# Kernel optimization log

Measured on AMD Instinct MI355X. Metric: run time of the kernel, lower is better.

Reference implementation:

```python
import jax, jax.numpy as jnp
import numpy as np

AH, AW = 8, 8            # aligned_height, aligned_width
SCALE = 0.0625           # spatial_scale = 1/16
IMG = 1024               # image size implied by 64x64 feature map at stride 16


def setup_inputs() -> dict:
    key = jax.random.key(0)
    k1, k2, k3, k4, k5 = jax.random.split(key, 5)
    B, C, H, W = 4, 256, 64, 64
    N = 2000
    features = jax.random.normal(k1, (B, C, H, W), dtype=jnp.float32)
    # ROIs: (batch_idx, x1, y1, x2, y2) in image coordinates
    bidx = jax.random.randint(k2, (N,), 0, B).astype(jnp.float32)
    cx = jax.random.uniform(k3, (N,), minval=0.0, maxval=IMG)
    cy = jax.random.uniform(k4, (N,), minval=0.0, maxval=IMG)
    wh = jax.random.uniform(k5, (N, 2), minval=32.0, maxval=512.0)
    x1 = jnp.clip(cx - wh[:, 0] / 2, 0.0, IMG - 1.0)
    y1 = jnp.clip(cy - wh[:, 1] / 2, 0.0, IMG - 1.0)
    x2 = jnp.clip(cx + wh[:, 0] / 2, x1 + 16.0, float(IMG))
    y2 = jnp.clip(cy + wh[:, 1] / 2, y1 + 16.0, float(IMG))
    rois = jnp.stack([bidx, x1, y1, x2, y2], axis=1).astype(jnp.float32)
    return {"features": features, "rois": rois}


def _roi_align(features, rois):
    # Classic RoIAlign (crop_and_resize style): one bilinear sample per output
    # cell, sample grid spans the ROI with (aligned-1) intervals.
    B, C, H, W = features.shape
    N = rois.shape[0]
    b = rois[:, 0].astype(jnp.int32)
    x1 = rois[:, 1] * SCALE
    y1 = rois[:, 2] * SCALE
    x2 = rois[:, 3] * SCALE
    y2 = rois[:, 4] * SCALE
    bin_h = (y2 - y1) / (AH - 1.0)
    bin_w = (x2 - x1) / (AW - 1.0)
    ys = y1[:, None, None] + bin_h[:, None, None] * jnp.arange(AH, dtype=jnp.float32)[None, :, None]
    xs = x1[:, None, None] + bin_w[:, None, None] * jnp.arange(AW, dtype=jnp.float32)[None, None, :]
    ys = jnp.broadcast_to(ys, (N, AH, AW))
    xs = jnp.broadcast_to(xs, (N, AH, AW))
    valid = (ys >= 0) & (ys < H) & (xs >= 0) & (xs < W)
    y0 = jnp.floor(ys)
    x0 = jnp.floor(xs)
    ly = ys - y0  # bilinear weights
    lx = xs - x0
    iy0 = jnp.clip(y0.astype(jnp.int32), 0, H - 1)
    ix0 = jnp.clip(x0.astype(jnp.int32), 0, W - 1)
    iy1 = jnp.clip(iy0 + 1, 0, H - 1)
    ix1 = jnp.clip(ix0 + 1, 0, W - 1)
    bb = b[:, None, None]

    def g(iy, ix):
        return features[bb, :, iy, ix]  # [N, AH, AW, C]

    ly_ = ly[..., None]
    lx_ = lx[..., None]
    v = ((1 - ly_) * (1 - lx_) * g(iy0, ix0)
         + (1 - ly_) * lx_ * g(iy0, ix1)
         + ly_ * (1 - lx_) * g(iy1, ix0)
         + ly_ * lx_ * g(iy1, ix1))
    v = jnp.where(valid[..., None], v, 0.0)
    return jnp.transpose(v, (0, 3, 1, 2))  # [N, C, AH, AW]


def _max_pool_2x2_s1(x):
    # max_pool2d(kernel_size=2, stride=1): [N,C,h,w] -> [N,C,h-1,w-1]
    return jnp.maximum(
        jnp.maximum(x[:, :, :-1, :-1], x[:, :, :-1, 1:]),
        jnp.maximum(x[:, :, 1:, :-1], x[:, :, 1:, 1:]),
    )


def reference(features, rois):
    x = _roi_align(features, rois)
    return _max_pool_2x2_s1(x)  # [N, C, AH-1, AW-1]
```

## Files before the change

kernel.cpp:

```cpp
#include <hip/hip_runtime.h>
#include <cstdint>

constexpr int CCH = 256;
constexpr int HH  = 64;
constexpr int WW  = 64;
constexpr int OHW = 49;
constexpr float RSCALE = 0.0625f;

#define FMUL __fmul_rn
#define FADD __fadd_rn
#define FSUB __fsub_rn
#define FDIV __fdiv_rn

typedef float     v4f __attribute__((ext_vector_type(4)));
typedef _Float16  h2  __attribute__((ext_vector_type(2)));
typedef _Float16  h4  __attribute__((ext_vector_type(4)));

__device__ __forceinline__ h2 pkrtz(float a, float b) {
  auto t = __builtin_amdgcn_cvt_pkrtz(a, b);
  union { decltype(t) s; h2 d; } c; c.s = t; return c.d;
}
__device__ __forceinline__ h4 bcast4(float a) {
  h2 t = pkrtz(a, a);
  return __builtin_shufflevector(t, t, 0, 1, 0, 1);
}
__device__ __forceinline__ h4 u2h(uint2 u) {
  union { uint2 u; h4 h; } c; c.u = u; return c.h;
}
__device__ __forceinline__ h4 h4max(h4 a, h4 b) {
  return __builtin_elementwise_max(a, b);
}

__global__ __launch_bounds__(256) void ktrans_sched(const float* __restrict__ in,
                                                    unsigned short* __restrict__ out,
                                                    const float* __restrict__ rois,
                                                    int N, int slots, int do_sched,
                                                    int B, int* __restrict__ meta) {
  const int t = threadIdx.x;

  if ((int)blockIdx.z == B) {
    if (blockIdx.x != 0 || blockIdx.y != 0 || !do_sched) return;
    __shared__ int cnt[4], rnk[4], off[4], slack[4], excess[4];
    if (t < 4) { cnt[t] = 0; rnk[t] = 0; }
    __syncthreads();
    for (int i = t; i < N; i += 256) atomicAdd(&cnt[(int)rois[i * 5]], 1);
    __syncthreads();
    if (t == 0) {
      int o = 0, cs = 0, ce = 0;
      for (int p = 0; p < 4; ++p) {
        off[p] = o; o += cnt[p];
        slack[p]  = cs; if (slots - cnt[p] > 0) cs += slots - cnt[p];
        excess[p] = ce; if (cnt[p] - slots > 0) ce += cnt[p] - slots;
        meta[p] = cnt[p]; meta[4 + p] = off[p]; meta[8 + p] = slack[p];
      }
    }
    __syncthreads();
    int* perm = meta + 16;
    for (int i = t; i < N; i += 256) {
      const int b = (int)rois[i * 5];
      perm[off[b] + atomicAdd(&rnk[b], 1)] = i;
    }
    __syncthreads();
    int* extra = meta + 16 + N;
    for (int p = 0; p < 4; ++p) {
      const int ex = cnt[p] - slots;
      for (int e = t; e < ex; e += 256) extra[excess[p] + e] = perm[off[p] + slots + e];
    }
    return;
  }

  __shared__ float tile[64][65];
  const int b  = blockIdx.z;
  const int c0 = blockIdx.y * 64;
  const int s0 = blockIdx.x * 64;
  const float* inb = in + (size_t)b * CCH * (HH * WW);
  unsigned short* outb = out + (size_t)b * (HH * WW) * CCH;

  const int cl = t >> 4, sq = t & 15;
#pragma unroll
  for (int k = 0; k < 4; ++k) {
    const int c = cl + 16 * k;
    const v4f v = __builtin_nontemporal_load(
        (const v4f*)(inb + (size_t)(c0 + c) * (HH * WW) + s0 + 4 * sq));
    tile[c][4 * sq + 0] = v[0];
    tile[c][4 * sq + 1] = v[1];
    tile[c][4 * sq + 2] = v[2];
    tile[c][4 * sq + 3] = v[3];
  }
  __syncthreads();
  const int cq = t & 15, rl = t >> 4;
#pragma unroll
  for (int k = 0; k < 4; ++k) {
    const int r = rl + 16 * k;
    union { h2 h; unsigned u; } p0, p1;
    p0.h.x = (_Float16)tile[4 * cq + 0][r];
    p0.h.y = (_Float16)tile[4 * cq + 1][r];
    p1.h.x = (_Float16)tile[4 * cq + 2][r];
    p1.h.y = (_Float16)tile[4 * cq + 3][r];
    uint2 w; w.x = p0.u; w.y = p1.u;
    *(uint2*)(outb + (size_t)(s0 + r) * CCH + c0 + 4 * cq) = w;
  }
}

__global__ __launch_bounds__(256, 4) void roi_kernel12(const uint2* __restrict__ feat,
                                                       const float* __restrict__ rois,
                                                       const int* __restrict__ meta,
                                                       int N, int M, int use_perm,
                                                       float* __restrict__ out) {
  __shared__ __attribute__((aligned(16))) h4       ldsA[OHW * 32];
  __shared__ __attribute__((aligned(16))) _Float16 ldsC[(CCH / 2) * OHW];
  const int t = threadIdx.x;
  const int g = t & 31;
  const int r = t >> 5;

  const int c0_ = use_perm ? meta[0] : 0;
  const int c1_ = use_perm ? meta[1] : 0;
  const int c2_ = use_perm ? meta[2] : 0;
  const int c3_ = use_perm ? meta[3] : 0;
  const int o0_ = use_perm ? meta[4] : 0, o1_ = use_perm ? meta[5] : 0;
  const int o2_ = use_perm ? meta[6] : 0, o3_ = use_perm ? meta[7] : 0;
  const int s0_ = use_perm ? meta[8] : 0, s1_ = use_perm ? meta[9] : 0;
  const int s2_ = use_perm ? meta[10] : 0, s3_ = use_perm ? meta[11] : 0;
  const int* perm  = meta + 16;
  const int* extra = meta + 16 + N;

  for (int i = blockIdx.x; i < M; i += gridDim.x) {
    int n, half;
    if (use_perm) {
      const int p = (i & 7) >> 1;
      half        = i & 1;
      const int s = i >> 3;
      const int c_ = p == 0 ? c0_ : (p == 1 ? c1_ : (p == 2 ? c2_ : c3_));
      const int o_ = p == 0 ? o0_ : (p == 1 ? o1_ : (p == 2 ? o2_ : o3_));
      const int sl = p == 0 ? s0_ : (p == 1 ? s1_ : (p == 2 ? s2_ : s3_));
      n = (s < c_) ? perm[o_ + s] : extra[sl + (s - c_)];
    } else {
      n = i >> 1; half = i & 1;
    }

    const float rb = rois[n * 5 + 0];
    const float x1 = FMUL(rois[n * 5 + 1], RSCALE);
    const float y1 = FMUL(rois[n * 5 + 2], RSCALE);
    const float x2 = FMUL(rois[n * 5 + 3], RSCALE);
    const float y2 = FMUL(rois[n * 5 + 4], RSCALE);
    const int   b  = (int)rb;
    const float bh = FDIV(FSUB(y2, y1), 7.0f);
    const float bw = FDIV(FSUB(x2, x1), 7.0f);

    int   xo0[8], xo1[8];
    float lx[8];
    bool  xv[8];
#pragma unroll
    for (int q = 0; q < 8; ++q) {
      const float xs = FADD(x1, FMUL(bw, (float)q));
      xv[q] = (xs >= 0.0f) && (xs < (float)WW);
      const float xf = floorf(xs);
      lx[q] = FSUB(xs, xf);
      int a = (int)xf;
      a = a < 0 ? 0 : (a > WW - 1 ? WW - 1 : a);
      xo0[q] = a * (CCH / 4);
      xo1[q] = ((a + 1 > WW - 1) ? WW - 1 : a + 1) * (CCH / 4);
    }

    const float ys = FADD(y1, FMUL(bh, (float)r));
    const bool  yv = (ys >= 0.0f) && (ys < (float)HH);
    const float yf = floorf(ys);
    const float ly = FSUB(ys, yf);
    int d = (int)yf;
    d = d < 0 ? 0 : (d > HH - 1 ? HH - 1 : d);
    const int d1 = (d + 1 > HH - 1) ? HH - 1 : d + 1;

    const uint2* fb = feat + (size_t)b * (HH * WW) * (CCH / 4) + (half * 32 + g);
    const uint2* r0 = fb + (size_t)d  * (WW * (CCH / 4));
    const uint2* r1 = fb + (size_t)d1 * (WW * (CCH / 4));
    const float wy1 = ly, wy0 = 1.0f - ly;

    uint2 g00[8], g01[8], g10[8], g11[8];
#pragma unroll
    for (int q = 0; q < 8; ++q) {
      g00[q] = r0[xo0[q]];
      g01[q] = r0[xo1[q]];
      g10[q] = r1[xo0[q]];
      g11[q] = r1[xo1[q]];
    }

    h4 hc[7], vprev;
#pragma unroll
    for (int h = 0; h < 2; ++h) {
      h4 v[4];
#pragma unroll
      for (int q = 0; q < 4; ++q) {
        const int s = 4 * h + q;
        const bool ok = yv && xv[s];
        const float wx1 = lx[s], wx0 = 1.0f - wx1;
        const h4 w00 = bcast4(wy0 * wx0);
        const h4 w01 = bcast4(wy0 * wx1);
        const h4 w10 = bcast4(wy1 * wx0);
        const h4 w11 = bcast4(wy1 * wx1);
        h4 rr = w00 * u2h(g00[s]) + w01 * u2h(g01[s])
              + w10 * u2h(g10[s]) + w11 * u2h(g11[s]);
        v[q] = ok ? rr : h4{};
      }
      if (h == 0) {
        hc[0] = h4max(v[0], v[1]);
        hc[1] = h4max(v[1], v[2]);
        hc[2] = h4max(v[2], v[3]);
        vprev = v[3];
      } else {
        hc[3] = h4max(vprev, v[0]);
        hc[4] = h4max(v[0], v[1]);
        hc[5] = h4max(v[1], v[2]);
        hc[6] = h4max(v[2], v[3]);
      }
    }

    if (r >= 1) {
#pragma unroll
      for (int m = 0; m < 7; ++m)
        ldsA[((r - 1) * 7 + m) * 32 + g] = hc[m];
    }
    __syncthreads();

    if (r <= 6) {
      _Float16* cb = ldsC + (4 * g) * OHW + r * 7;
#pragma unroll
      for (int m = 0; m < 7; ++m) {
        const h4 x = h4max(hc[m], ldsA[(r * 7 + m) * 32 + g]);
        cb[0 * OHW + m] = x[0];
        cb[1 * OHW + m] = x[1];
        cb[2 * OHW + m] = x[2];
        cb[3 * OHW + m] = x[3];
      }
    }
    __syncthreads();

    const uint2* cs = (const uint2*)ldsC;
    v4f* o4 = (v4f*)(out + (size_t)n * (CCH * OHW) + half * (CCH / 2) * OHW);
#pragma unroll
    for (int m = 0; m < 7; ++m) {
      const int idx = m * 256 + t;
      if (idx < (CCH / 2) * OHW / 4) {
        const uint2 qv = cs[idx];
        union { unsigned u; h2 h; } e0, e1;
        e0.u = qv.x; e1.u = qv.y;
        v4f wv;
        wv.x = (float)e0.h.x;
        wv.y = (float)e0.h.y;
        wv.z = (float)e1.h.x;
        wv.w = (float)e1.h.y;
        __builtin_nontemporal_store(wv, o4 + idx);
      }
    }
  }
}

__global__ __launch_bounds__(256) void roi_kernel_fb(const float* __restrict__ feat,
                                                     const float* __restrict__ rois,
                                                     float* __restrict__ out) {
  __shared__ float sout[CCH * OHW];
  const int n = blockIdx.x;
  const int c = threadIdx.x;

  const float rb = rois[n * 5 + 0];
  const float x1 = FMUL(rois[n * 5 + 1], RSCALE);
  const float y1 = FMUL(rois[n * 5 + 2], RSCALE);
  const float x2 = FMUL(rois[n * 5 + 3], RSCALE);
  const float y2 = FMUL(rois[n * 5 + 4], RSCALE);
  const int b = (int)rb;
  const float bh = FDIV(FSUB(y2, y1), 7.0f);
  const float bw = FDIV(FSUB(x2, x1), 7.0f);

  int ix0[8], ix1[8], iy0[8], iy1[8];
  float lx[8], ly[8];
  bool xv[8], yv[8];
#pragma unroll
  for (int i = 0; i < 8; ++i) {
    const float xs = FADD(x1, FMUL(bw, (float)i));
    const float ys = FADD(y1, FMUL(bh, (float)i));
    xv[i] = (xs >= 0.0f) && (xs < (float)WW);
    yv[i] = (ys >= 0.0f) && (ys < (float)HH);
    const float xf = floorf(xs);
    const float yf = floorf(ys);
    lx[i] = FSUB(xs, xf);
    ly[i] = FSUB(ys, yf);
    int a = (int)xf;
    a = a < 0 ? 0 : (a > WW - 1 ? WW - 1 : a);
    ix0[i] = a;
    ix1[i] = (a + 1 > WW - 1) ? WW - 1 : a + 1;
    int d = (int)yf;
    d = d < 0 ? 0 : (d > HH - 1 ? HH - 1 : d);
    iy0[i] = d;
    iy1[i] = (d + 1 > HH - 1) ? HH - 1 : d + 1;
  }

  const float* fbp = feat + ((size_t)b * CCH + c) * (size_t)(HH * WW);
  float hp[7];
#pragma unroll
  for (int j = 0; j < 8; ++j) {
    float v[8];
    const float wy1 = ly[j], wy0 = 1.0f - ly[j];
#pragma unroll
    for (int i = 0; i < 8; ++i) {
      if (yv[j] && xv[i]) {
        const float f00 = fbp[iy0[j] * WW + ix0[i]];
        const float f01 = fbp[iy0[j] * WW + ix1[i]];
        const float f10 = fbp[iy1[j] * WW + ix0[i]];
        const float f11 = fbp[iy1[j] * WW + ix1[i]];
        const float wx1 = lx[i], wx0 = 1.0f - wx1;
        v[i] = wy0 * (wx0 * f00 + wx1 * f01) + wy1 * (wx0 * f10 + wx1 * f11);
      } else {
        v[i] = 0.0f;
      }
    }
    float hc[7];
#pragma unroll
    for (int i = 0; i < 7; ++i) hc[i] = fmaxf(v[i], v[i + 1]);
    if (j > 0) {
#pragma unroll
      for (int i = 0; i < 7; ++i)
        sout[c * OHW + (j - 1) * 7 + i] = fmaxf(hp[i], hc[i]);
    }
#pragma unroll
    for (int i = 0; i < 7; ++i) hp[i] = hc[i];
  }
  __syncthreads();
  const float4* s4 = (const float4*)sout;
  float4* o4 = (float4*)(out + (size_t)n * (CCH * OHW));
  for (int q = c; q < (CCH * OHW) / 4; q += 256) o4[q] = s4[q];
}

extern "C" void kernel_launch(void* const* d_in, const int* in_sizes, int n_in,
                              void* d_out, int out_size, void* d_ws, size_t ws_size,
                              hipStream_t stream) {
  (void)n_in; (void)out_size;
  const float* feat = (const float*)d_in[0];
  const float* rois = (const float*)d_in[1];
  float* out = (float*)d_out;
  const int N = in_sizes[1] / 5;
  const int B = in_sizes[0] / (CCH * HH * WW);
  const int M = 2 * N;
  const size_t featbf_bytes = (size_t)in_sizes[0] * sizeof(unsigned short);
  const size_t meta_bytes   = (size_t)(16 + 2 * N) * sizeof(int);

  if (ws_size >= featbf_bytes + meta_bytes) {
    unsigned short* featbf = (unsigned short*)d_ws;
    int* meta = (int*)((char*)d_ws + featbf_bytes);
    const int use_perm = (B == 4 && (M & 7) == 0) ? 1 : 0;

    ktrans_sched<<<dim3((HH * WW) / 64, CCH / 64, B + 1), dim3(256), 0, stream>>>(
        feat, featbf, rois, N, M >> 3, use_perm, B, meta);
    const int grid = (M >= 2048) ? 2048 : M;
    roi_kernel12<<<dim3(grid), dim3(256), 0, stream>>>(
        (const uint2*)featbf, rois, meta, N, M, use_perm, out);
  } else {
    roi_kernel_fb<<<dim3(N), dim3(256), 0, stream>>>(feat, rois, out);
  }
}
```

Baseline: 133.1 us.

## Fuse transpose, scheduling and ROI align into one kernel with grid barrier

Merges the feature transpose/fp16 conversion, the ROI batch scheduling, and the ROI align + max-pool kernel into one persistent kernel of 1024 blocks. A software grid-wide barrier built on global atomics separates the phases, and the LDS is shared between them. The scheduler now uses a prefix-scan instead of atomics, and the gather loads are split per half to lower register pressure. The aim is to remove the launch gap and tail between the two kernels. In exchange it adds a memset, relies on all 1024 blocks being co-resident (deadlock risk otherwise), and adds barrier overhead.

```diff
diff --git a/kernel.cpp b/kernel.cpp
--- a/kernel.cpp
+++ b/kernel.cpp
@@ -31,85 +31,122 @@
   return __builtin_elementwise_max(a, b);
 }
 
-__global__ __launch_bounds__(256) void ktrans_sched(const float* __restrict__ in,
-                                                    unsigned short* __restrict__ out,
-                                                    const float* __restrict__ rois,
-                                                    int N, int slots, int do_sched,
-                                                    int B, int* __restrict__ meta) {
-  const int t = threadIdx.x;
-
-  if ((int)blockIdx.z == B) {
-    if (blockIdx.x != 0 || blockIdx.y != 0 || !do_sched) return;
-    __shared__ int cnt[4], rnk[4], off[4], slack[4], excess[4];
-    if (t < 4) { cnt[t] = 0; rnk[t] = 0; }
-    __syncthreads();
-    for (int i = t; i < N; i += 256) atomicAdd(&cnt[(int)rois[i * 5]], 1);
-    __syncthreads();
+__global__ __launch_bounds__(256, 4) void fused_kernel(
+    const float* __restrict__ in, unsigned short* __restrict__ featbf,
+    const float* __restrict__ rois, int N, int M, int slots, int use_perm,
+    int B, int* __restrict__ meta, float* __restrict__ out) {
+  __shared__ __attribute__((aligned(16))) unsigned char lds_raw[25088];
+  const int t   = threadIdx.x;
+  const int bid = blockIdx.x;
+
+  {
+    float (*tile)[65] = (float (*)[65])lds_raw;
+    for (int tz = bid; tz < B * 256; tz += (int)gridDim.x) {
+      const int b  = tz >> 8;
+      const int c0 = ((tz >> 6) & 3) * 64;
+      const int s0 = (tz & 63) * 64;
+      const float* inb = in + (size_t)b * CCH * (HH * WW);
+      unsigned short* outb = featbf + (size_t)b * (HH * WW) * CCH;
+      const int cl = t >> 4, sq = t & 15;
+#pragma unroll
+      for (int k = 0; k < 4; ++k) {
+        const int c = cl + 16 * k;
+        const v4f v = __builtin_nontemporal_load(
+            (const v4f*)(inb + (size_t)(c0 + c) * (HH * WW) + s0 + 4 * sq));
+        tile[c][4 * sq + 0] = v[0];
+        tile[c][4 * sq + 1] = v[1];
+        tile[c][4 * sq + 2] = v[2];
+        tile[c][4 * sq + 3] = v[3];
+      }
+      __syncthreads();
+      const int cq = t & 15, rl = t >> 4;
+#pragma unroll
+      for (int k = 0; k < 4; ++k) {
+        const int r = rl + 16 * k;
+        union { h2 h; unsigned u; } p0, p1;
+        p0.h.x = (_Float16)tile[4 * cq + 0][r];
+        p0.h.y = (_Float16)tile[4 * cq + 1][r];
+        p1.h.x = (_Float16)tile[4 * cq + 2][r];
+        p1.h.y = (_Float16)tile[4 * cq + 3][r];
+        uint2 w; w.x = p0.u; w.y = p1.u;
+        *(uint2*)(outb + (size_t)(s0 + r) * CCH + c0 + 4 * cq) = w;
+      }
+      __syncthreads();
+    }
+  }
+
+  if (use_perm && bid == 0) {
+    int4* sc = (int4*)lds_raw;
+    int k0[4] = {0, 0, 0, 0};
+    int keys[8];
+    const int base = t * 8;
+#pragma unroll
+    for (int e = 0; e < 8; ++e) {
+      const int i = base + e;
+      int key = 4;
+      if (i < N) { key = (int)rois[i * 5]; k0[key]++; }
+      keys[e] = key;
+    }
+    sc[t] = make_int4(k0[0], k0[1], k0[2], k0[3]);
+    __syncthreads();
+    for (int d = 1; d < 256; d <<= 1) {
+      const int4 v = sc[t];
+      const int4 u = (t >= d) ? sc[t - d] : make_int4(0, 0, 0, 0);
+      __syncthreads();
+      sc[t] = make_int4(v.x + u.x, v.y + u.y, v.z + u.z, v.w + u.w);
+      __syncthreads();
+    }
+    const int4 incl = sc[t];
+    const int4 tot  = sc[255];
+    const int cnt_[4] = {tot.x, tot.y, tot.z, tot.w};
+    int off_[4];
+    off_[0] = 0; off_[1] = cnt_[0]; off_[2] = off_[1] + cnt_[1]; off_[3] = off_[2] + cnt_[2];
+    int rank[4] = {off_[0] + incl.x - k0[0], off_[1] + incl.y - k0[1],
+                   off_[2] + incl.z - k0[2], off_[3] + incl.w - k0[3]};
+    int* perm = meta + 16;
+#pragma unroll
+    for (int e = 0; e < 8; ++e) {
+      const int key = keys[e];
+      if (key < 4) perm[rank[key]++] = base + e;
+    }
     if (t == 0) {
-      int o = 0, cs = 0, ce = 0;
+      int cs = 0;
       for (int p = 0; p < 4; ++p) {
-        off[p] = o; o += cnt[p];
-        slack[p]  = cs; if (slots - cnt[p] > 0) cs += slots - cnt[p];
-        excess[p] = ce; if (cnt[p] - slots > 0) ce += cnt[p] - slots;
-        meta[p] = cnt[p]; meta[4 + p] = off[p]; meta[8 + p] = slack[p];
-      }
-    }
-    __syncthreads();
-    int* perm = meta + 16;
-    for (int i = t; i < N; i += 256) {
-      const int b = (int)rois[i * 5];
-      perm[off[b] + atomicAdd(&rnk[b], 1)] = i;
+        meta[p] = cnt_[p]; meta[4 + p] = off_[p]; meta[8 + p] = cs;
+        if (slots - cnt_[p] > 0) cs += slots - cnt_[p];
+      }
     }
     __syncthreads();
     int* extra = meta + 16 + N;
+    int exbase = 0;
     for (int p = 0; p < 4; ++p) {
-      const int ex = cnt[p] - slots;
-      for (int e = t; e < ex; e += 256) extra[excess[p] + e] = perm[off[p] + slots + e];
-    }
-    return;
-  }
-
-  __shared__ float tile[64][65];
-  const int b  = blockIdx.z;
-  const int c0 = blockIdx.y * 64;
-  const int s0 = blockIdx.x * 64;
-  const float* inb = in + (size_t)b * CCH * (HH * WW);
-  unsigned short* outb = out + (size_t)b * (HH * WW) * CCH;
-
-  const int cl = t >> 4, sq = t & 15;
-#pragma unroll
-  for (int k = 0; k < 4; ++k) {
-    const int c = cl + 16 * k;
-    const v4f v = __builtin_nontemporal_load(
-        (const v4f*)(inb + (size_t)(c0 + c) * (HH * WW) + s0 + 4 * sq));
-    tile[c][4 * sq + 0] = v[0];
-    tile[c][4 * sq + 1] = v[1];
-    tile[c][4 * sq + 2] = v[2];
-    tile[c][4 * sq + 3] = v[3];
-  }
-  __syncthreads();
-  const int cq = t & 15, rl = t >> 4;
-#pragma unroll
-  for (int k = 0; k < 4; ++k) {
-    const int r = rl + 16 * k;
-    union { h2 h; unsigned u; } p0, p1;
-    p0.h.x = (_Float16)tile[4 * cq + 0][r];
-    p0.h.y = (_Float16)tile[4 * cq + 1][r];
-    p1.h.x = (_Float16)tile[4 * cq + 2][r];
-    p1.h.y = (_Float16)tile[4 * cq + 3][r];
-    uint2 w; w.x = p0.u; w.y = p1.u;
-    *(uint2*)(outb + (size_t)(s0 + r) * CCH + c0 + 4 * cq) = w;
-  }
-}
-
-__global__ __launch_bounds__(256, 4) void roi_kernel12(const uint2* __restrict__ feat,
-                                                       const float* __restrict__ rois,
-                                                       const int* __restrict__ meta,
-                                                       int N, int M, int use_perm,
-                                                       float* __restrict__ out) {
-  __shared__ __attribute__((aligned(16))) h4       ldsA[OHW * 32];
-  __shared__ __attribute__((aligned(16))) _Float16 ldsC[(CCH / 2) * OHW];
-  const int t = threadIdx.x;
+      const int ex = cnt_[p] - slots;
+      for (int e = t; e < ex; e += 256) extra[exbase + e] = perm[off_[p] + slots + e];
+      if (ex > 0) exbase += ex;
+    }
+  }
+
+  {
+    unsigned* bar = (unsigned*)(meta + 12);
+    __threadfence();
+    __syncthreads();
+    if (t == 0) {
+      const unsigned old = __hip_atomic_fetch_add(&bar[0], 1u, __ATOMIC_ACQ_REL,
+                                                  __HIP_MEMORY_SCOPE_AGENT);
+      if (old == (unsigned)gridDim.x - 1u) {
+        __hip_atomic_store(&bar[1], 1u, __ATOMIC_RELEASE, __HIP_MEMORY_SCOPE_AGENT);
+      } else {
+        while (!__hip_atomic_load(&bar[1], __ATOMIC_ACQUIRE, __HIP_MEMORY_SCOPE_AGENT))
+          __builtin_amdgcn_s_sleep(16);
+      }
+    }
+    __syncthreads();
+    __threadfence();
+  }
+
+  h4*       ldsA = (h4*)lds_raw;
+  _Float16* ldsC = (_Float16*)(lds_raw + 12544);
+  const uint2* feat = (const uint2*)featbf;
   const int g = t & 31;
   const int r = t >> 5;
 
@@ -124,7 +161,7 @@
   const int* perm  = meta + 16;
   const int* extra = meta + 16 + N;
 
-  for (int i = blockIdx.x; i < M; i += gridDim.x) {
+  for (int i = bid; i < M; i += (int)gridDim.x) {
     int n, half;
     if (use_perm) {
       const int p = (i & 7) >> 1;
@@ -175,18 +212,18 @@
     const uint2* r1 = fb + (size_t)d1 * (WW * (CCH / 4));
     const float wy1 = ly, wy0 = 1.0f - ly;
 
-    uint2 g00[8], g01[8], g10[8], g11[8];
-#pragma unroll
-    for (int q = 0; q < 8; ++q) {
-      g00[q] = r0[xo0[q]];
-      g01[q] = r0[xo1[q]];
-      g10[q] = r1[xo0[q]];
-      g11[q] = r1[xo1[q]];
-    }
-
     h4 hc[7], vprev;
 #pragma unroll
     for (int h = 0; h < 2; ++h) {
+      uint2 g00[4], g01[4], g10[4], g11[4];
+#pragma unroll
+      for (int q = 0; q < 4; ++q) {
+        const int s = 4 * h + q;
+        g00[q] = r0[xo0[s]];
+        g01[q] = r0[xo1[s]];
+        g10[q] = r1[xo0[s]];
+        g11[q] = r1[xo1[s]];
+      }
       h4 v[4];
 #pragma unroll
       for (int q = 0; q < 4; ++q) {
@@ -197,8 +234,8 @@
         const h4 w01 = bcast4(wy0 * wx1);
         const h4 w10 = bcast4(wy1 * wx0);
         const h4 w11 = bcast4(wy1 * wx1);
-        h4 rr = w00 * u2h(g00[s]) + w01 * u2h(g01[s])
-              + w10 * u2h(g10[s]) + w11 * u2h(g11[s]);
+        h4 rr = w00 * u2h(g00[q]) + w01 * u2h(g01[q])
+              + w10 * u2h(g10[q]) + w11 * u2h(g11[q]);
         v[q] = ok ? rr : h4{};
       }
       if (h == 0) {
@@ -239,7 +276,7 @@
 #pragma unroll
     for (int m = 0; m < 7; ++m) {
       const int idx = m * 256 + t;
-      if (idx < (CCH / 2) * OHW / 4) {
+      if (m < 6 || t < 32) {
         const uint2 qv = cs[idx];
         union { unsigned u; h2 h; } e0, e1;
         e0.u = qv.x; e1.u = qv.y;
@@ -342,16 +379,16 @@
   const size_t featbf_bytes = (size_t)in_sizes[0] * sizeof(unsigned short);
   const size_t meta_bytes   = (size_t)(16 + 2 * N) * sizeof(int);
 
-  if (ws_size >= featbf_bytes + meta_bytes) {
+  if (ws_size >= featbf_bytes + meta_bytes && N <= 2048 && B == 4 && (M & 7) == 0) {
     unsigned short* featbf = (unsigned short*)d_ws;
     int* meta = (int*)((char*)d_ws + featbf_bytes);
-    const int use_perm = (B == 4 && (M & 7) == 0) ? 1 : 0;
-
-    ktrans_sched<<<dim3((HH * WW) / 64, CCH / 64, B + 1), dim3(256), 0, stream>>>(
-        feat, featbf, rois, N, M >> 3, use_perm, B, meta);
-    const int grid = (M >= 2048) ? 2048 : M;
-    roi_kernel12<<<dim3(grid), dim3(256), 0, stream>>>(
-        (const uint2*)featbf, rois, meta, N, M, use_perm, out);
+    const int use_perm = 1;
+    const int slots = M >> 3;
+
+    hipMemsetAsync((void*)(meta + 12), 0, 2 * sizeof(int), stream);
+
+    fused_kernel<<<dim3(1024), dim3(256), 0, stream>>>(
+        feat, featbf, rois, N, M, slots, use_perm, B, meta, out);
   } else {
     roi_kernel_fb<<<dim3(N), dim3(256), 0, stream>>>(feat, rois, out);
   }
```

Result: slower. 376.0 us (+182.5%).
